# Performance work log

Measured on AMD Instinct MI355X. Metric: run time of the kernel, lower is better.

The kernel has to match this reference:

```python
import jax, jax.numpy as jnp
import numpy as np

D_NIBBLE = 16
NIBBLE_VALUES = 16
NUM_NIBBLES = 8


def _build_tables():
    num_entries = NIBBLE_VALUES * NIBBLE_VALUES * 2  # 512
    input_dim = 2 * D_NIBBLE + 2                     # 34
    W1 = np.zeros((input_dim, num_entries), dtype=np.float32)
    W2_sum = np.zeros((num_entries, D_NIBBLE), dtype=np.float32)
    W2_carry = np.zeros((num_entries, 2), dtype=np.float32)
    for a in range(NIBBLE_VALUES):
        for b in range(NIBBLE_VALUES):
            for c in range(2):
                k = a * 32 + b * 2 + c
                W1[a, k] = 1.0
                W1[D_NIBBLE + b, k] = 1.0
                W1[2 * D_NIBBLE + c, k] = 1.0
                total = a + b + c
                W2_sum[k, total % 16] = 1.0
                W2_carry[k, 1 if total >= 16 else 0] = 1.0
    return jnp.asarray(W1), jnp.asarray(W2_sum), jnp.asarray(W2_carry)


def setup_inputs() -> dict:
    key = jax.random.key(0)
    k1, k2 = jax.random.split(key)
    B = 32768
    a_nibbles = jax.random.uniform(k1, (B, NUM_NIBBLES, 32), dtype=jnp.float32)
    b_nibbles = jax.random.uniform(k2, (B, NUM_NIBBLES, 32), dtype=jnp.float32)
    W1, W2_sum, W2_carry = _build_tables()
    threshold = jnp.float32(2.5)
    return {"a_nibbles": a_nibbles, "b_nibbles": b_nibbles,
            "W1": W1, "W2_sum": W2_sum, "W2_carry": W2_carry,
            "threshold": threshold}


def reference(a_nibbles, b_nibbles, W1, W2_sum, W2_carry, threshold):
    # a_nibbles, b_nibbles: [B, 8, 32]; first 16 feats = value one-hot, rest = pos
    B = a_nibbles.shape[0]
    carry0 = jnp.zeros((B, 2), a_nibbles.dtype).at[:, 0].set(1.0)  # carry=0 one-hot
    a_steps = jnp.swapaxes(a_nibbles, 0, 1)  # [8, B, 32]
    b_steps = jnp.swapaxes(b_nibbles, 0, 1)

    def step(carry, ab):
        a, b = ab  # [B, 32] each
        x = jnp.concatenate([a[:, :D_NIBBLE], b[:, :D_NIBBLE], carry], axis=-1)  # [B,34]
        scores = x @ W1                                     # [B,512]
        weights = jax.nn.softmax((scores - threshold) * 10.0, axis=-1)
        result = weights @ W2_sum                           # [B,16]
        new_carry = weights @ W2_carry                      # [B,2]
        out = jnp.concatenate([result, a[:, D_NIBBLE:]], axis=-1)  # [B,32]
        return new_carry, out

    _, outs = jax.lax.scan(step, carry0, (a_steps, b_steps))  # outs: [8, B, 32]
    return jnp.swapaxes(outs, 0, 1)  # [B, 8, 32]
```

## Files before the change

### kernel.cpp

```cpp
#include <hip/hip_runtime.h>


#define LOG2E10 14.426950408889634f

#if __has_builtin(__builtin_amdgcn_exp2f)
#define EXP2F(x) __builtin_amdgcn_exp2f(x)
#else
#define EXP2F(x) exp2f(x)
#endif

#if __has_builtin(__builtin_amdgcn_rcpf)
#define RCPF(x) __builtin_amdgcn_rcpf(x)
#else
#define RCPF(x) (1.0f / (x))
#endif

#define EBZ(x) ebz[(x) + 12]

template <int CTRL>
__device__ __forceinline__ float qdpp(float x) {
    return __int_as_float(__builtin_amdgcn_update_dpp(
        0, __float_as_int(x), CTRL, 0xF, 0xF, true));
}

template <int OFF>
__device__ __forceinline__ float swz32(float x) {
    return __int_as_float(__builtin_amdgcn_ds_swizzle(__float_as_int(x), OFF));
}

__global__ __launch_bounds__(256, 4) void AdditionFFN_kernel(
    const float4* __restrict__ A, const float4* __restrict__ Bv,
    float4* __restrict__ O, int nRows)
{
    const int T = threadIdx.x;
    const int r = T & 31;
    const int c = r & 3;
    const int s = r >> 2;
    const int row = blockIdx.x * 8 + (T >> 5);
    if (row >= nRows) return;
    const float4* a4 = A + (size_t)row * 64;
    const float4* b4 = Bv + (size_t)row * 64;
    float4* o4 = O + (size_t)row * 64;

    const float4 av = a4[s * 8 + c];
    const float4 bv = b4[s * 8 + c];
    const float4 pv = a4[s * 8 + 4 + c];
    o4[s * 8 + 4 + c] = pv;

    float ea_own[4] = { EXP2F(av.x * LOG2E10), EXP2F(av.y * LOG2E10),
                        EXP2F(av.z * LOG2E10), EXP2F(av.w * LOG2E10) };
    float eb_own[4] = { EXP2F(bv.x * LOG2E10), EXP2F(bv.y * LOG2E10),
                        EXP2F(bv.z * LOG2E10), EXP2F(bv.w * LOG2E10) };

    float ea[16];
    #pragma unroll
    for (int m = 0; m < 4; ++m) {
        ea[m]      = qdpp<0x00>(ea_own[m]);
        ea[4 + m]  = qdpp<0x55>(ea_own[m]);
        ea[8 + m]  = qdpp<0xAA>(ea_own[m]);
        ea[12 + m] = qdpp<0xFF>(ea_own[m]);
    }

    float ebr[4][4];
    #pragma unroll
    for (int m = 0; m < 4; ++m) {
        ebr[0][m] = eb_own[m];
        ebr[1][m] = qdpp<0x39>(eb_own[m]);
        ebr[2][m] = qdpp<0x4E>(eb_own[m]);
        ebr[3][m] = qdpp<0x93>(eb_own[m]);
    }

    float ebz[28];
    #pragma unroll
    for (int x = -12; x <= 15; ++x) {
        float vsh = ebr[(x >> 2) & 3][x & 3];
        bool keep;
        if (x >= 0 && x <= 3)  keep = true;
        else if (x < 0)        keep = (c >= ((3 - x) >> 2));
        else                   keep = (c <= ((15 - x) >> 2));
        EBZ(x) = keep ? vsh : 0.0f;
    }

    float ulo[5], uhi[5];
    #pragma unroll
    for (int i = 0; i < 5; ++i) {
        float acc = 0.0f;
        const int amax = (i + 11 < 15) ? (i + 11) : 15;
        #pragma unroll
        for (int a = 0; a <= amax; ++a) {
            acc = __builtin_fmaf(ea[a], EBZ(i - 1 - a), acc);
        }
        ulo[i] = acc;
    }
    #pragma unroll
    for (int i = 0; i < 5; ++i) {
        float acc = 0.0f;
        #pragma unroll
        for (int a = i; a < 16; ++a) {
            acc = __builtin_fmaf(ea[a], EBZ(i + 15 - a), acc);
        }
        uhi[i] = acc;
    }

    float sap = (ea_own[0] + ea_own[1]) + (ea_own[2] + ea_own[3]);
    sap += qdpp<0xB1>(sap);
    sap += qdpp<0x4E>(sap);
    float sbp = (eb_own[0] + eb_own[1]) + (eb_own[2] + eb_own[3]);
    sbp += qdpp<0xB1>(sbp);
    sbp += qdpp<0x4E>(sbp);
    float Nm = sap * sbp;
    float rN = RCPF(Nm);
    rN = rN * (2.0f - Nm * rN);

    float hi0p = (uhi[1] + uhi[2]) + (uhi[3] + uhi[4]);
    hi0p += qdpp<0xB1>(hi0p);
    hi0p += qdpp<0x4E>(hi0p);
    float hs = hi0p * rN;
    float ms = qdpp<0x00>(uhi[0]) * rN;

    float h0 = swz32<0x003>(hs), m0 = swz32<0x003>(ms);
    float h1 = swz32<0x083>(hs), m1 = swz32<0x083>(ms);
    float h2 = swz32<0x103>(hs), m2 = swz32<0x103>(ms);
    float h3 = swz32<0x183>(hs), m3 = swz32<0x183>(ms);
    float h4 = swz32<0x203>(hs), m4 = swz32<0x203>(ms);
    float h5 = swz32<0x283>(hs), m5 = swz32<0x283>(ms);
    float h6 = swz32<0x303>(hs), m6 = swz32<0x303>(ms);
    float h7 = swz32<0x383>(hs), m7 = swz32<0x383>(ms);

    float c1 = 0.0f, wmine = 0.0f;
#define CARRY_STEP(K, HK, MK)                                        \
    {                                                                \
        float e0 = EXP2F((1.0f - c1) * LOG2E10);                     \
        float e1 = EXP2F(c1 * LOG2E10);                              \
        float E = e0 + e1;                                           \
        float rE = RCPF(E);                                          \
        rE = rE * (2.0f - E * rE);                                   \
        float w = e1 * rE;                                           \
        if (s == K) wmine = w;                                       \
        c1 = __builtin_fmaf(w, MK, HK);                              \
        c1 = fminf(fmaxf(c1, 0.0f), 1.0f);                           \
    }
    CARRY_STEP(0, h0, m0)
    CARRY_STEP(1, h1, m1)
    CARRY_STEP(2, h2, m2)
    CARRY_STEP(3, h3, m3)
    CARRY_STEP(4, h4, m4)
    CARRY_STEP(5, h5, m5)
    CARRY_STEP(6, h6, m6)
    CARRY_STEP(7, h7, m7)
#undef CARRY_STEP

    float vm1 = ulo[0] + uhi[0];
    float v0 = ulo[1] + uhi[1];
    float v1 = ulo[2] + uhi[2];
    float v2 = ulo[3] + uhi[3];
    float v3 = ulo[4] + uhi[4];
    float4 rr;
    rr.x = __builtin_fmaf(wmine, vm1 - v0, v0) * rN;
    rr.y = __builtin_fmaf(wmine, v0 - v1, v1) * rN;
    rr.z = __builtin_fmaf(wmine, v1 - v2, v2) * rN;
    rr.w = __builtin_fmaf(wmine, v2 - v3, v3) * rN;
    o4[s * 8 + c] = rr;
}

extern "C" void kernel_launch(void* const* d_in, const int* in_sizes, int n_in,
                              void* d_out, int out_size, void* d_ws, size_t ws_size,
                              hipStream_t stream) {
    (void)n_in; (void)out_size; (void)d_ws; (void)ws_size;
    const int nRows = in_sizes[0] / 256;
    const float4* A  = (const float4*)d_in[0];
    const float4* Bv = (const float4*)d_in[1];
    float4* O = (float4*)d_out;
    int blocks = (nRows + 7) / 8;
    AdditionFFN_kernel<<<blocks, 256, 0, stream>>>(A, Bv, O, nRows);
}
```

Before: 109.5 us.

## Compute cyclic convolution directly and derive carry sums from prefix sums

```diff
diff --git a/kernel.cpp b/kernel.cpp
--- a/kernel.cpp
+++ b/kernel.cpp
@@ -15,7 +15,11 @@
 #define RCPF(x) (1.0f / (x))
 #endif
 
-#define EBZ(x) ebz[(x) + 12]
+#if __has_builtin(__builtin_amdgcn_fmed3f)
+#define CLAMP01(x) __builtin_amdgcn_fmed3f((x), 0.0f, 1.0f)
+#else
+#define CLAMP01(x) fminf(fmaxf((x), 0.0f), 1.0f)
+#endif
 
 template <int CTRL>
 __device__ __forceinline__ float qdpp(float x) {
@@ -45,12 +49,13 @@
     const float4 av = a4[s * 8 + c];
     const float4 bv = b4[s * 8 + c];
     const float4 pv = a4[s * 8 + 4 + c];
-    o4[s * 8 + 4 + c] = pv;
 
     float ea_own[4] = { EXP2F(av.x * LOG2E10), EXP2F(av.y * LOG2E10),
                         EXP2F(av.z * LOG2E10), EXP2F(av.w * LOG2E10) };
     float eb_own[4] = { EXP2F(bv.x * LOG2E10), EXP2F(bv.y * LOG2E10),
                         EXP2F(bv.z * LOG2E10), EXP2F(bv.w * LOG2E10) };
+
+    o4[s * 8 + 4 + c] = pv;
 
     float ea[16];
     #pragma unroll
@@ -70,53 +75,51 @@
         ebr[3][m] = qdpp<0x93>(eb_own[m]);
     }
 
-    float ebz[28];
+    float v[4];
     #pragma unroll
-    for (int x = -12; x <= 15; ++x) {
-        float vsh = ebr[(x >> 2) & 3][x & 3];
-        bool keep;
-        if (x >= 0 && x <= 3)  keep = true;
-        else if (x < 0)        keep = (c >= ((3 - x) >> 2));
-        else                   keep = (c <= ((15 - x) >> 2));
-        EBZ(x) = keep ? vsh : 0.0f;
-    }
-
-    float ulo[5], uhi[5];
-    #pragma unroll
-    for (int i = 0; i < 5; ++i) {
-        float acc = 0.0f;
-        const int amax = (i + 11 < 15) ? (i + 11) : 15;
-        #pragma unroll
-        for (int a = 0; a <= amax; ++a) {
-            acc = __builtin_fmaf(ea[a], EBZ(i - 1 - a), acc);
-        }
-        ulo[i] = acc;
-    }
-    #pragma unroll
-    for (int i = 0; i < 5; ++i) {
+    for (int k = 0; k < 4; ++k) {
         float acc = 0.0f;
         #pragma unroll
-        for (int a = i; a < 16; ++a) {
-            acc = __builtin_fmaf(ea[a], EBZ(i + 15 - a), acc);
+        for (int a = 0; a < 16; ++a) {
+            const int x = k - a;
+            acc = __builtin_fmaf(ea[a], ebr[(x >> 2) & 3][x & 3], acc);
         }
-        uhi[i] = acc;
+        v[k] = acc;
     }
+    float vm1 = qdpp<0x93>(v[3]);
 
     float sap = (ea_own[0] + ea_own[1]) + (ea_own[2] + ea_own[3]);
     sap += qdpp<0xB1>(sap);
     sap += qdpp<0x4E>(sap);
-    float sbp = (eb_own[0] + eb_own[1]) + (eb_own[2] + eb_own[3]);
-    sbp += qdpp<0xB1>(sbp);
-    sbp += qdpp<0x4E>(sbp);
-    float Nm = sap * sbp;
+    float pb = (eb_own[0] + eb_own[1]) + (eb_own[2] + eb_own[3]);
+    float r1 = qdpp<0x39>(pb);
+    float r2 = qdpp<0x4E>(pb);
+    float r3 = qdpp<0x93>(pb);
+    float Sb = ((pb + r1) + (r2 + r3));
+    float Nm = sap * Sb;
     float rN = RCPF(Nm);
     rN = rN * (2.0f - Nm * rN);
 
-    float hi0p = (uhi[1] + uhi[2]) + (uhi[3] + uhi[4]);
-    hi0p += qdpp<0xB1>(hi0p);
-    hi0p += qdpp<0x4E>(hi0p);
-    float hs = hi0p * rN;
-    float ms = qdpp<0x00>(uhi[0]) * rN;
+    float FA = (c < 3 ? r1 : 0.0f) + (c < 2 ? r2 : 0.0f) + (c < 1 ? r3 : 0.0f);
+    float t1 = eb_own[3];
+    float t2 = t1 + eb_own[2];
+    float t3 = t2 + eb_own[1];
+    float ss1 = t3 + FA;
+    float ss2 = t2 + FA;
+    float ss3 = t1 + FA;
+    float mFA = qdpp<0x1B>(FA);
+    float mS3 = qdpp<0x1B>(ss3);
+    float mS2 = qdpp<0x1B>(ss2);
+    float mS1 = qdpp<0x1B>(ss1);
+    float hp = __builtin_fmaf(ea_own[0], mFA,
+               __builtin_fmaf(ea_own[1], mS3,
+               __builtin_fmaf(ea_own[2], mS2, ea_own[3] * mS1)));
+    hp += qdpp<0xB1>(hp);
+    hp += qdpp<0x4E>(hp);
+
+    float u15 = qdpp<0xFF>(v[3]);
+    float hs = hp * rN;
+    float ms = u15 * rN;
 
     float h0 = swz32<0x003>(hs), m0 = swz32<0x003>(ms);
     float h1 = swz32<0x083>(hs), m1 = swz32<0x083>(ms);
@@ -130,15 +133,12 @@
     float c1 = 0.0f, wmine = 0.0f;
 #define CARRY_STEP(K, HK, MK)                                        \
     {                                                                \
-        float e0 = EXP2F((1.0f - c1) * LOG2E10);                     \
-        float e1 = EXP2F(c1 * LOG2E10);                              \
-        float E = e0 + e1;                                           \
-        float rE = RCPF(E);                                          \
-        rE = rE * (2.0f - E * rE);                                   \
-        float w = e1 * rE;                                           \
+        float t = __builtin_fmaf(c1, -2.0f * LOG2E10, LOG2E10);      \
+        float d = 1.0f + EXP2F(t);                                   \
+        float w = RCPF(d);                                           \
         if (s == K) wmine = w;                                       \
         c1 = __builtin_fmaf(w, MK, HK);                              \
-        c1 = fminf(fmaxf(c1, 0.0f), 1.0f);                           \
+        c1 = CLAMP01(c1);                                            \
     }
     CARRY_STEP(0, h0, m0)
     CARRY_STEP(1, h1, m1)
@@ -150,16 +150,11 @@
     CARRY_STEP(7, h7, m7)
 #undef CARRY_STEP
 
-    float vm1 = ulo[0] + uhi[0];
-    float v0 = ulo[1] + uhi[1];
-    float v1 = ulo[2] + uhi[2];
-    float v2 = ulo[3] + uhi[3];
-    float v3 = ulo[4] + uhi[4];
     float4 rr;
-    rr.x = __builtin_fmaf(wmine, vm1 - v0, v0) * rN;
-    rr.y = __builtin_fmaf(wmine, v0 - v1, v1) * rN;
-    rr.z = __builtin_fmaf(wmine, v1 - v2, v2) * rN;
-    rr.w = __builtin_fmaf(wmine, v2 - v3, v3) * rN;
+    rr.x = __builtin_fmaf(wmine, vm1 - v[0], v[0]) * rN;
+    rr.y = __builtin_fmaf(wmine, v[0] - v[1], v[1]) * rN;
+    rr.z = __builtin_fmaf(wmine, v[1] - v[2], v[2]) * rN;
+    rr.w = __builtin_fmaf(wmine, v[2] - v[3], v[3]) * rN;
     o4[s * 8 + c] = rr;
 }
 
```

Result: no change. 108.7 us (-0.7%).
